# Kernel tuning notes

Measured on AMD Instinct MI355X. Metric: run time of the kernel, lower is better.

The kernel has to match this reference:

```python
import jax, jax.numpy as jnp
import numpy as np

DIM = 2048
CTX_DIM = 4096
NUM_HEADS = 16
HEAD_DIM = DIM // NUM_HEADS
EPS = 1e-6


def _rms_norm(x, weight, eps=EPS):
    # RMSNorm over last dim with learned weight (native dtype path for fp32)
    var = jnp.mean(jnp.square(x), axis=-1, keepdims=True)
    return x * jax.lax.rsqrt(var + eps) * weight


def setup_inputs() -> dict:
    key = jax.random.key(0)
    ks = jax.random.split(key, 12)
    B, L, S = 1, 8192, 512
    sd_q = 1.0 / np.sqrt(DIM)
    sd_c = 1.0 / np.sqrt(CTX_DIM)
    return {
        "x": jax.random.normal(ks[0], (B, L, DIM), dtype=jnp.float32),
        "context": jax.random.normal(ks[1], (B, S, CTX_DIM), dtype=jnp.float32),
        "Wq": jax.random.normal(ks[2], (DIM, DIM), dtype=jnp.float32) * sd_q,
        "bq": jax.random.normal(ks[3], (DIM,), dtype=jnp.float32) * 0.01,
        "Wk": jax.random.normal(ks[4], (CTX_DIM, DIM), dtype=jnp.float32) * sd_c,
        "bk": jax.random.normal(ks[5], (DIM,), dtype=jnp.float32) * 0.01,
        "Wv": jax.random.normal(ks[6], (CTX_DIM, DIM), dtype=jnp.float32) * sd_c,
        "bv": jax.random.normal(ks[7], (DIM,), dtype=jnp.float32) * 0.01,
        "Wo": jax.random.normal(ks[8], (DIM, DIM), dtype=jnp.float32) * sd_q,
        "bo": jax.random.normal(ks[9], (DIM,), dtype=jnp.float32) * 0.01,
        "g_q": jnp.ones((DIM,), dtype=jnp.float32),
        "g_k": jnp.ones((DIM,), dtype=jnp.float32),
    }


def reference(x, context, Wq, bq, Wk, bk, Wv, bv, Wo, bo, g_q, g_k):
    B, L, C = x.shape
    S = context.shape[1]
    # QKV projections + RMSNorm on Q,K (over full model dim, pre head split)
    q = _rms_norm(x @ Wq + bq, g_q)           # [B, L, C]
    k = _rms_norm(context @ Wk + bk, g_k)     # [B, S, C]
    v = context @ Wv + bv                     # [B, S, C]
    # split heads
    q = q.reshape(B, L, NUM_HEADS, HEAD_DIM)
    k = k.reshape(B, S, NUM_HEADS, HEAD_DIM)
    v = v.reshape(B, S, NUM_HEADS, HEAD_DIM)
    # non-causal SDPA
    scale = 1.0 / np.sqrt(HEAD_DIM)
    scores = jnp.einsum("blhd,bshd->bhls", q, k) * scale
    probs = jax.nn.softmax(scores, axis=-1)
    attn = jnp.einsum("bhls,bshd->blhd", probs, v).reshape(B, L, C)
    return attn @ Wo + bo
```

## Files before the change

kernel.cpp:

```cpp
#include <hip/hip_runtime.h>
#include <hip/hip_bf16.h>
#include <stdint.h>

#define L_SEQ 8192
#define S_SEQ 512
#define DIM   2048
#define CTX   4096
#define NH    16
#define HD    128

typedef __bf16 bf16_t;
typedef bf16_t bf16x8 __attribute__((ext_vector_type(8)));
typedef float  f32x4_t __attribute__((ext_vector_type(4)));
typedef float  f32x16_t __attribute__((ext_vector_type(16)));

__device__ __forceinline__ ushort f2b(float f) {
  union { float f; uint32_t u; } v; v.f = f;
  uint32_t u = v.u;
  uint32_t r = (u + 0x7fffu + ((u >> 16) & 1u)) >> 16;
  return (ushort)r;
}
__device__ __forceinline__ uint32_t pk2(float a, float b) {
  return (uint32_t)f2b(a) | ((uint32_t)f2b(b) << 16);
}
__device__ __forceinline__ float b2f(ushort u) {
  union { uint32_t u; float f; } v; v.u = ((uint32_t)u) << 16;
  return v.f;
}
__device__ __forceinline__ void gll16(const ushort* g, ushort* l) {
  __builtin_amdgcn_global_load_lds((const __attribute__((address_space(1))) void*)g,
                                   (__attribute__((address_space(3))) void*)l, 16, 0, 0);
}

__global__ __launch_bounds__(256) void k_cast(const float* __restrict__ in,
                                              ushort* __restrict__ out) {
  const size_t i = ((size_t)blockIdx.x * 256 + threadIdx.x) * 8;
  float4 a = *(const float4*)(in + i);
  float4 b = *(const float4*)(in + i + 4);
  uint4 r;
  r.x = pk2(a.x, a.y); r.y = pk2(a.z, a.w);
  r.z = pk2(b.x, b.y); r.w = pk2(b.z, b.w);
  *(uint4*)(out + i) = r;
}

__global__ __launch_bounds__(256) void k_tcast(const float* __restrict__ src,
                                               ushort* __restrict__ dst, int K, int N) {
  __shared__ float t[32][33];
  int tx = threadIdx.x, ty = threadIdx.y;
  int n0 = blockIdx.x * 32, k0 = blockIdx.y * 32;
#pragma unroll
  for (int i = 0; i < 4; i++)
    t[ty + 8 * i][tx] = src[(size_t)(k0 + ty + 8 * i) * N + n0 + tx];
  __syncthreads();
#pragma unroll
  for (int i = 0; i < 4; i++)
    dst[(size_t)(n0 + ty + 8 * i) * K + k0 + tx] = f2b(t[tx][ty + 8 * i]);
}

__global__ __launch_bounds__(256) void k_rmsnorm(const ushort* __restrict__ in,
                                                 ushort* __restrict__ out,
                                                 const float* __restrict__ g, float scale) {
  const int row = blockIdx.x, tid = threadIdx.x;
  uint4 v = *(const uint4*)(in + (size_t)row * DIM + tid * 8);
  const uint32_t* vu = (const uint32_t*)&v;
  float f[8];
#pragma unroll
  for (int i = 0; i < 4; i++) {
    f[2 * i]     = b2f((ushort)(vu[i] & 0xffffu));
    f[2 * i + 1] = b2f((ushort)(vu[i] >> 16));
  }
  float s = 0.f;
#pragma unroll
  for (int i = 0; i < 8; i++) s += f[i] * f[i];
#pragma unroll
  for (int off = 32; off; off >>= 1) s += __shfl_down(s, off);
  __shared__ float wsum[4];
  __shared__ float rtot;
  if ((tid & 63) == 0) wsum[tid >> 6] = s;
  __syncthreads();
  if (tid == 0)
    rtot = rsqrtf((wsum[0] + wsum[1] + wsum[2] + wsum[3]) * (1.0f / DIM) + 1e-6f);
  __syncthreads();
  const float rms = rtot * scale;
  const float* gp = g + tid * 8;
  float4 g0 = *(const float4*)gp, g1 = *(const float4*)(gp + 4);
  ushort r[8];
  r[0] = f2b(f[0] * rms * g0.x); r[1] = f2b(f[1] * rms * g0.y);
  r[2] = f2b(f[2] * rms * g0.z); r[3] = f2b(f[3] * rms * g0.w);
  r[4] = f2b(f[4] * rms * g1.x); r[5] = f2b(f[5] * rms * g1.y);
  r[6] = f2b(f[6] * rms * g1.z); r[7] = f2b(f[7] * rms * g1.w);
  *(uint4*)(out + (size_t)row * DIM + tid * 8) = *(uint4*)r;
}

template <int OUT_MODE>
__global__ __launch_bounds__(512, 2) void k_gemm256(const ushort* __restrict__ A,
                                                    const ushort* __restrict__ Bt,
                                                    const float* __restrict__ bias,
                                                    void* __restrict__ outp,
                                                    int M, int N, int K) {
  __shared__ __align__(16) ushort lds[65536];
  const int tid = threadIdx.x;
  const int l = tid & 63, wid = tid >> 6;
  const int wm = wid >> 2, wn = wid & 3;
  const int lr = l & 15, lq = l >> 4;

  const int nwg = gridDim.x * gridDim.y;
  const int bid = blockIdx.y * gridDim.x + blockIdx.x;
  const int swz = (bid & 7) * (nwg >> 3) + (bid >> 3);
  const int m0 = (swz / gridDim.x) * 256, n0 = (swz % gridDim.x) * 256;

  f32x4_t acc[8][4];
#pragma unroll
  for (int i = 0; i < 8; i++)
#pragma unroll
    for (int j = 0; j < 4; j++) acc[i][j] = f32x4_t{0.f, 0.f, 0.f, 0.f};

  const int srow = l >> 3;
  const int schunk = ((l & 7) ^ (srow & 7)) * 8;
  auto stage = [&](int buf, int tile, int mat, int h) {
    const ushort* gp = mat ? Bt : A;
    const int rn0 = mat ? n0 : m0;
    const size_t r0 = (size_t)(rn0 + h * 128 + wid * 8 + srow);
    const ushort* g0 = gp + r0 * K + tile * 64 + schunk;
    ushort* l0 = &lds[buf * 32768 + mat * 16384 + (h * 128 + wid * 8) * 64];
    gll16(g0, l0);
    gll16(g0 + (size_t)64 * K, l0 + 64 * 64);
  };

  auto rdA = [&](int buf, int mf, int ks) -> bf16x8 {
    const int R = wm * 128 + mf * 16 + lr;
    return *(const bf16x8*)(&lds[buf * 32768 + R * 64 + (((ks * 4 + lq) ^ (R & 7)) * 8)]);
  };
  auto rdB = [&](int buf, int nf, int ks) -> bf16x8 {
    const int R = wn * 64 + nf * 16 + lr;
    return *(const bf16x8*)(&lds[buf * 32768 + 16384 + R * 64 + (((ks * 4 + lq) ^ (R & 7)) * 8)]);
  };

  const int NT = K >> 6;
  stage(0, 0, 0, 0); stage(0, 0, 0, 1); stage(0, 0, 1, 0); stage(0, 0, 1, 1);

  bf16x8 a[4][2], a2[4][2], b[2][2], b2[2][2];
  for (int kt = 0; kt < NT; kt++) {
    const int cur = kt & 1, nxt = cur ^ 1;
    const bool pf = (kt + 1 < NT);
    if (pf) {
      stage(nxt, kt + 1, 0, 0); stage(nxt, kt + 1, 0, 1);
      stage(nxt, kt + 1, 1, 0); stage(nxt, kt + 1, 1, 1);
      asm volatile("s_waitcnt vmcnt(8)" ::: "memory");
    } else {
      asm volatile("s_waitcnt vmcnt(0)" ::: "memory");
    }
    __builtin_amdgcn_sched_barrier(0);
    __builtin_amdgcn_s_barrier();
    __builtin_amdgcn_sched_barrier(0);
#pragma unroll
    for (int mf = 0; mf < 4; mf++) { a[mf][0] = rdA(cur, mf, 0); a[mf][1] = rdA(cur, mf, 1); }
#pragma unroll
    for (int nf = 0; nf < 2; nf++) { b[nf][0] = rdB(cur, nf, 0); b[nf][1] = rdB(cur, nf, 1); }
    __builtin_amdgcn_s_setprio(1);
#pragma unroll
    for (int mf = 0; mf < 4; mf++)
#pragma unroll
      for (int nf = 0; nf < 2; nf++) {
        acc[mf][nf] = __builtin_amdgcn_mfma_f32_16x16x32_bf16(a[mf][0], b[nf][0], acc[mf][nf], 0, 0, 0);
        acc[mf][nf] = __builtin_amdgcn_mfma_f32_16x16x32_bf16(a[mf][1], b[nf][1], acc[mf][nf], 0, 0, 0);
      }
    __builtin_amdgcn_s_setprio(0);
    __builtin_amdgcn_sched_barrier(0);
    __builtin_amdgcn_s_barrier();
    __builtin_amdgcn_sched_barrier(0);
#pragma unroll
    for (int mf = 0; mf < 4; mf++) { a2[mf][0] = rdA(cur, mf + 4, 0); a2[mf][1] = rdA(cur, mf + 4, 1); }
    __builtin_amdgcn_sched_barrier(0);
    __builtin_amdgcn_s_barrier();
    __builtin_amdgcn_sched_barrier(0);
    __builtin_amdgcn_s_setprio(1);
#pragma unroll
    for (int mf = 0; mf < 4; mf++)
#pragma unroll
      for (int nf = 0; nf < 2; nf++) {
        acc[mf + 4][nf] = __builtin_amdgcn_mfma_f32_16x16x32_bf16(a2[mf][0], b[nf][0], acc[mf + 4][nf], 0, 0, 0);
        acc[mf + 4][nf] = __builtin_amdgcn_mfma_f32_16x16x32_bf16(a2[mf][1], b[nf][1], acc[mf + 4][nf], 0, 0, 0);
      }
    __builtin_amdgcn_s_setprio(0);
    __builtin_amdgcn_sched_barrier(0);
    __builtin_amdgcn_s_barrier();
    __builtin_amdgcn_sched_barrier(0);
#pragma unroll
    for (int nf = 0; nf < 2; nf++) { b2[nf][0] = rdB(cur, nf + 2, 0); b2[nf][1] = rdB(cur, nf + 2, 1); }
    __builtin_amdgcn_sched_barrier(0);
    __builtin_amdgcn_s_barrier();
    __builtin_amdgcn_sched_barrier(0);
    __builtin_amdgcn_s_setprio(1);
#pragma unroll
    for (int mf = 0; mf < 4; mf++)
#pragma unroll
      for (int nf = 0; nf < 2; nf++) {
        acc[mf + 4][nf + 2] = __builtin_amdgcn_mfma_f32_16x16x32_bf16(a2[mf][0], b2[nf][0], acc[mf + 4][nf + 2], 0, 0, 0);
        acc[mf + 4][nf + 2] = __builtin_amdgcn_mfma_f32_16x16x32_bf16(a2[mf][1], b2[nf][1], acc[mf + 4][nf + 2], 0, 0, 0);
      }
    __builtin_amdgcn_s_setprio(0);
    __builtin_amdgcn_sched_barrier(0);
    __builtin_amdgcn_s_barrier();
    __builtin_amdgcn_sched_barrier(0);
    __builtin_amdgcn_s_setprio(1);
#pragma unroll
    for (int mf = 0; mf < 4; mf++)
#pragma unroll
      for (int nf = 0; nf < 2; nf++) {
        acc[mf][nf + 2] = __builtin_amdgcn_mfma_f32_16x16x32_bf16(a[mf][0], b2[nf][0], acc[mf][nf + 2], 0, 0, 0);
        acc[mf][nf + 2] = __builtin_amdgcn_mfma_f32_16x16x32_bf16(a[mf][1], b2[nf][1], acc[mf][nf + 2], 0, 0, 0);
      }
    __builtin_amdgcn_s_setprio(0);
    __builtin_amdgcn_sched_barrier(0);
    __builtin_amdgcn_s_barrier();
    __builtin_amdgcn_sched_barrier(0);
  }

#pragma unroll
  for (int nf = 0; nf < 4; nf++) {
    const int col = n0 + wn * 64 + nf * 16 + lr;
    const float bv = bias[col];
#pragma unroll
    for (int mf = 0; mf < 8; mf++) {
#pragma unroll
      for (int r = 0; r < 4; r++) {
        const int row = m0 + wm * 128 + mf * 16 + lq * 4 + r;
        const float v = acc[mf][nf][r] + bv;
        if constexpr (OUT_MODE == 0)
          ((float*)outp)[(size_t)row * N + col] = v;
        else
          ((ushort*)outp)[(size_t)row * N + col] = f2b(v);
      }
    }
  }
}

__global__ __launch_bounds__(256) void k_gemmkv(const ushort* __restrict__ A,
                                                const ushort* __restrict__ Bt,
                                                const float* __restrict__ biasK,
                                                const float* __restrict__ biasV,
                                                ushort* __restrict__ outK,
                                                ushort* __restrict__ outVt) {
  __shared__ __align__(16) ushort As[4][128 * 32];
  __shared__ __align__(16) ushort Bs[4][64 * 32];
  const int tid = threadIdx.x;
  const int l = tid & 63, wid = tid >> 6;
  const int wr = wid >> 1, wc = wid & 1;
  const int lr = l & 15, lq = l >> 4;
  const int K = CTX, M = S_SEQ;

  const int bid = blockIdx.x;
  const int swz = (bid & 7) * 32 + (bid >> 3);
  const int n0 = (swz >> 2) * 64, m0 = (swz & 3) * 128;

  f32x4_t acc[4][2];
#pragma unroll
  for (int i = 0; i < 4; i++)
#pragma unroll
    for (int j = 0; j < 2; j++) acc[i][j] = f32x4_t{0.f, 0.f, 0.f, 0.f};

  const int srow = l >> 2;
  const int schunk = ((l & 3) ^ ((srow >> 1) & 3)) * 8;
  const ushort* gA = A  + (size_t)(m0 + srow) * K + schunk;
  const ushort* gB = Bt + (size_t)(n0 + wid * 16 + srow) * K + schunk;

  auto stage = [&](int buf, int kt) {
    const int ko = kt * 32;
    gll16(gA + (size_t)(wid * 16) * K + ko,      &As[buf][(wid * 16) * 32]);
    gll16(gA + (size_t)(64 + wid * 16) * K + ko, &As[buf][(64 + wid * 16) * 32]);
    gll16(gB + ko,                               &Bs[buf][(wid * 16) * 32]);
  };
  auto rdA = [&](int buf, int mi) -> bf16x8 {
    const int R = wr * 64 + mi * 16 + lr;
    return *(const bf16x8*)(&As[buf][R * 32 + ((lq ^ ((R >> 1) & 3)) * 8)]);
  };
  auto rdB = [&](int buf, int ni) -> bf16x8 {
    const int R = wc * 32 + ni * 16 + lr;
    return *(const bf16x8*)(&Bs[buf][R * 32 + ((lq ^ ((R >> 1) & 3)) * 8)]);
  };

  const int NT = K >> 5;
  stage(0, 0); stage(1, 1); stage(2, 2);
  for (int t = 0; t < NT; t++) {
    const int cur = t & 3;
    if (t + 3 < NT) { stage((t + 3) & 3, t + 3); asm volatile("s_waitcnt vmcnt(9)" ::: "memory"); }
    else if (t + 2 < NT) { asm volatile("s_waitcnt vmcnt(6)" ::: "memory"); }
    else if (t + 1 < NT) { asm volatile("s_waitcnt vmcnt(3)" ::: "memory"); }
    else                 { asm volatile("s_waitcnt vmcnt(0)" ::: "memory"); }
    __builtin_amdgcn_sched_barrier(0);
    __builtin_amdgcn_s_barrier();
    __builtin_amdgcn_sched_barrier(0);

    bf16x8 af[4], bfr[2];
#pragma unroll
    for (int mi = 0; mi < 4; mi++) af[mi] = rdA(cur, mi);
#pragma unroll
    for (int ni = 0; ni < 2; ni++) bfr[ni] = rdB(cur, ni);
    __builtin_amdgcn_s_setprio(1);
#pragma unroll
    for (int mi = 0; mi < 4; mi++)
#pragma unroll
      for (int ni = 0; ni < 2; ni++)
        acc[mi][ni] = __builtin_amdgcn_mfma_f32_16x16x32_bf16(af[mi], bfr[ni], acc[mi][ni], 0, 0, 0);
    __builtin_amdgcn_s_setprio(0);
    __builtin_amdgcn_sched_barrier(0);
    __builtin_amdgcn_s_barrier();
    __builtin_amdgcn_sched_barrier(0);
  }

#pragma unroll
  for (int mi = 0; mi < 4; mi++) {
#pragma unroll
    for (int ni = 0; ni < 2; ni++) {
      const int col = n0 + wc * 32 + ni * 16 + lr;
      const float bv = (col < DIM) ? biasK[col] : biasV[col - DIM];
#pragma unroll
      for (int r = 0; r < 4; r++) {
        const int row = m0 + wr * 64 + mi * 16 + lq * 4 + r;
        const float v = acc[mi][ni][r] + bv;
        if (col < DIM) outK[(size_t)row * DIM + col] = f2b(v);
        else           outVt[(size_t)(col - DIM) * M + row] = f2b(v);
      }
    }
  }
}

__global__ __launch_bounds__(256) void k_attn(const ushort* __restrict__ Qb,
                                              const ushort* __restrict__ Kb,
                                              const ushort* __restrict__ Vt,
                                              ushort* __restrict__ Ob) {
  __shared__ __align__(16) ushort smem[16384];
  ushort* Ks = smem;
  ushort* Vs = smem + 64 * 128;

  const int tid = threadIdx.x;
  const int l = tid & 63, wid = tid >> 6;
  const int lo = l & 31, hi = l >> 5;

  const int bid = blockIdx.x;
  const int swz = (bid & 7) * 128 + (bid >> 3);
  const int h = swz >> 6;
  const int q0 = (swz & 63) * 128 + wid * 32;

  bf16x8 qf[8];
  {
    const ushort* qp = Qb + (size_t)(q0 + lo) * DIM + h * HD + hi * 8;
#pragma unroll
    for (int ds = 0; ds < 8; ds++) qf[ds] = *(const bf16x8*)(qp + ds * 16);
  }

  f32x16_t o[4] = {};
  float m_run = -1e30f, l_run = 0.f;

  for (int kvb = 0; kvb < S_SEQ / 64; kvb++) {
    __syncthreads();
#pragma unroll
    for (int i = 0; i < 4; i++) {
      const int c = i * 256 + tid, row = c >> 4, cs = c & 15;
      gll16(Kb + (size_t)(kvb * 64 + row) * DIM + h * HD + ((cs ^ (row & 7)) * 8),
            Ks + c * 8);
    }
#pragma unroll
    for (int i = 0; i < 4; i++) {
      const int c = i * 256 + tid, row = c >> 3, cs = c & 7;
      gll16(Vt + (size_t)(h * HD + row) * S_SEQ + kvb * 64 + ((cs ^ (row & 7)) * 8),
            Vs + c * 8);
    }
    __syncthreads();

    f32x16_t sA = {}, sB = {};
#pragma unroll
    for (int ds = 0; ds < 8; ds++) {
      const int ch = ((hi + ds * 2) ^ (lo & 7)) * 8;
      bf16x8 kA = *(const bf16x8*)(Ks + lo * 128 + ch);
      bf16x8 kB = *(const bf16x8*)(Ks + (32 + lo) * 128 + ch);
      sA = __builtin_amdgcn_mfma_f32_32x32x16_bf16(kA, qf[ds], sA, 0, 0, 0);
      sB = __builtin_amdgcn_mfma_f32_32x32x16_bf16(kB, qf[ds], sB, 0, 0, 0);
    }

    float p[32];
#pragma unroll
    for (int i = 0; i < 16; i++) { p[i] = sA[i]; p[16 + i] = sB[i]; }
    float pm = p[0];
#pragma unroll
    for (int i = 1; i < 32; i++) pm = fmaxf(pm, p[i]);
    pm = fmaxf(pm, __shfl_xor(pm, 32));
    const float mn = fmaxf(m_run, pm);
    const float corr = __expf(m_run - mn);
    m_run = mn;
    float ps = 0.f;
#pragma unroll
    for (int i = 0; i < 32; i++) { p[i] = __expf(p[i] - mn); ps += p[i]; }
    ps += __shfl_xor(ps, 32);
    l_run = l_run * corr + ps;
#pragma unroll
    for (int nt = 0; nt < 4; nt++) o[nt] *= corr;

    uint32_t c[16];
#pragma unroll
    for (int j = 0; j < 16; j++) c[j] = pk2(p[2 * j], p[2 * j + 1]);
    bf16x8 pf[4];
#pragma unroll
    for (int s = 0; s < 4; s++) {
      const uint32_t ca = c[4 * s], cb = c[4 * s + 1], cc = c[4 * s + 2], cd = c[4 * s + 3];
      const uint32_t sa = __shfl_xor(ca, 32), sb = __shfl_xor(cb, 32);
      const uint32_t sc = __shfl_xor(cc, 32), sd = __shfl_xor(cd, 32);
      union { uint32_t u[4]; bf16x8 v; } f;
      f.u[0] = hi ? sc : ca; f.u[1] = hi ? sd : cb;
      f.u[2] = hi ? cc : sa; f.u[3] = hi ? cd : sb;
      pf[s] = f.v;
    }

#pragma unroll
    for (int nt = 0; nt < 4; nt++) {
      const int vrow = nt * 32 + lo;
#pragma unroll
      for (int s = 0; s < 4; s++) {
        bf16x8 vf = *(const bf16x8*)(Vs + vrow * 64 + (((s * 2 + hi) ^ (lo & 7)) * 8));
        o[nt] = __builtin_amdgcn_mfma_f32_32x32x16_bf16(vf, pf[s], o[nt], 0, 0, 0);
      }
    }
  }

  const float inv = 1.0f / l_run;
#pragma unroll
  for (int nt = 0; nt < 4; nt++) o[nt] *= inv;

  __syncthreads();
  float* tb = (float*)smem + wid * (32 * 33);
  const int q2 = l >> 1, dh = (l & 1) * 16;
#pragma unroll
  for (int nt = 0; nt < 4; nt++) {
#pragma unroll
    for (int r = 0; r < 16; r++)
      tb[lo * 33 + ((r & 3) + 8 * (r >> 2) + 4 * hi)] = o[nt][r];
    asm volatile("s_waitcnt lgkmcnt(0)" ::: "memory");
    __builtin_amdgcn_sched_barrier(0);
    ushort tmp[16];
#pragma unroll
    for (int j = 0; j < 16; j++) tmp[j] = f2b(tb[q2 * 33 + dh + j]);
    asm volatile("s_waitcnt lgkmcnt(0)" ::: "memory");
    __builtin_amdgcn_sched_barrier(0);
    const size_t oaddr = (size_t)(q0 + q2) * DIM + h * HD + nt * 32 + dh;
    *(uint4*)(Ob + oaddr) = *(uint4*)tmp;
    *(uint4*)(Ob + oaddr + 8) = *(uint4*)(tmp + 8);
  }
}

extern "C" void kernel_launch(void* const* d_in, const int* in_sizes, int n_in,
                              void* d_out, int out_size, void* d_ws, size_t ws_size,
                              hipStream_t stream) {
  const float* x   = (const float*)d_in[0];
  const float* ctx = (const float*)d_in[1];
  const float* Wq  = (const float*)d_in[2];
  const float* bq  = (const float*)d_in[3];
  const float* Wk  = (const float*)d_in[4];
  const float* bk  = (const float*)d_in[5];
  const float* Wv  = (const float*)d_in[6];
  const float* bv  = (const float*)d_in[7];
  const float* Wo  = (const float*)d_in[8];
  const float* bo  = (const float*)d_in[9];
  const float* gq  = (const float*)d_in[10];
  const float* gk  = (const float*)d_in[11];

  char* ws = (char*)d_ws;
  ushort* wqt   = (ushort*)(ws);
  ushort* wkt   = (ushort*)(ws + 8388608);
  ushort* wvt   = (ushort*)(ws + 25165824);
  ushort* wot   = (ushort*)(ws + 41943040);
  ushort* qb    = (ushort*)(ws + 50331648);
  ushort* kb    = (ushort*)(ws + 83886080);
  ushort* vt    = (ushort*)(ws + 85983232);
  ushort* xb    = (ushort*)(ws + 88080384);
  ushort* ctxb  = (ushort*)(ws + 88080384);
  ushort* qraw  = (ushort*)(ws + 121634816);
  ushort* kraw  = (ushort*)(ws + 121634816);
  ushort* attnb = (ushort*)(ws + 121634816);

  k_cast<<<L_SEQ * DIM / 8 / 256, 256, 0, stream>>>(x, xb);
  k_tcast<<<dim3(DIM / 32, DIM / 32), dim3(32, 8), 0, stream>>>(Wq, wqt, DIM, DIM);
  k_tcast<<<dim3(DIM / 32, CTX / 32), dim3(32, 8), 0, stream>>>(Wk, wkt, CTX, DIM);
  k_tcast<<<dim3(DIM / 32, CTX / 32), dim3(32, 8), 0, stream>>>(Wv, wvt, CTX, DIM);
  k_tcast<<<dim3(DIM / 32, DIM / 32), dim3(32, 8), 0, stream>>>(Wo, wot, DIM, DIM);

  k_gemm256<1><<<dim3(DIM / 256, L_SEQ / 256), 512, 0, stream>>>(xb, wqt, bq, qraw, L_SEQ, DIM, DIM);
  k_cast<<<S_SEQ * CTX / 8 / 256, 256, 0, stream>>>(ctx, ctxb);
  k_rmsnorm<<<L_SEQ, 256, 0, stream>>>(qraw, qb, gq, 0.08838834764831843f);
  k_gemmkv<<<256, 256, 0, stream>>>(ctxb, wkt, bk, bv, kraw, vt);
  k_rmsnorm<<<S_SEQ, 256, 0, stream>>>(kraw, kb, gk, 1.0f);
  k_attn<<<L_SEQ / 128 * NH, 256, 0, stream>>>(qb, kb, vt, attnb);
  k_gemm256<0><<<dim3(DIM / 256, L_SEQ / 256), 512, 0, stream>>>(attnb, wot, bo, d_out, L_SEQ, DIM, DIM);
}
```

Before: 338.4 us.

## Fuse fp32-to-bf16 cast of x into Q GEMM and double-buffer attention KV

The Q projection GEMM now reads fp32 x directly through registers, converts it to bf16 and writes it into LDS, so the separate cast kernel and its bf16 round trip through global memory go away. The attention kernel double-buffers its K/V tiles in LDS, prefetching the next block while the current one is computed. The price is extra register pressure and fp32 global traffic in the GEMM's A path, plus twice the LDS per attention block, which could lower occupancy.

Result: slower. 663.8 us (+96.2%).

```diff
diff --git a/kernel.cpp b/kernel.cpp
--- a/kernel.cpp
+++ b/kernel.cpp
@@ -92,7 +92,7 @@
   *(uint4*)(out + (size_t)row * DIM + tid * 8) = *(uint4*)r;
 }
 
-template <int OUT_MODE>
+template <int OUT_MODE, int AF32>
 __global__ __launch_bounds__(512, 2) void k_gemm256(const ushort* __restrict__ A,
                                                     const ushort* __restrict__ Bt,
                                                     const float* __restrict__ bias,
@@ -126,6 +126,27 @@
     gll16(g0, l0);
     gll16(g0 + (size_t)64 * K, l0 + 64 * 64);
   };
+  float4 ar[8];
+  auto loadA = [&](int tile) {
+    const float* Af = (const float*)A;
+#pragma unroll
+    for (int i = 0; i < 4; i++) {
+      const float* p = Af + (size_t)(m0 + i * 64 + wid * 8 + srow) * K + tile * 64 + schunk;
+      ar[2 * i]     = *(const float4*)p;
+      ar[2 * i + 1] = *(const float4*)(p + 4);
+    }
+  };
+  auto writeA = [&](int buf) {
+#pragma unroll
+    for (int i = 0; i < 4; i++) {
+      uint4 w;
+      w.x = pk2(ar[2 * i].x, ar[2 * i].y);
+      w.y = pk2(ar[2 * i].z, ar[2 * i].w);
+      w.z = pk2(ar[2 * i + 1].x, ar[2 * i + 1].y);
+      w.w = pk2(ar[2 * i + 1].z, ar[2 * i + 1].w);
+      *(uint4*)(&lds[buf * 32768 + (i * 64 + wid * 8 + srow) * 64 + (l & 7) * 8]) = w;
+    }
+  };
 
   auto rdA = [&](int buf, int mf, int ks) -> bf16x8 {
     const int R = wm * 128 + mf * 16 + lr;
@@ -137,18 +158,37 @@
   };
 
   const int NT = K >> 6;
-  stage(0, 0, 0, 0); stage(0, 0, 0, 1); stage(0, 0, 1, 0); stage(0, 0, 1, 1);
+  if constexpr (AF32) {
+    loadA(0);
+    stage(0, 0, 1, 0); stage(0, 0, 1, 1);
+    asm volatile("s_waitcnt vmcnt(4)" ::: "memory");
+    writeA(0);
+    asm volatile("s_waitcnt lgkmcnt(0)" ::: "memory");
+    __builtin_amdgcn_sched_barrier(0);
+  } else {
+    stage(0, 0, 0, 0); stage(0, 0, 0, 1); stage(0, 0, 1, 0); stage(0, 0, 1, 1);
+  }
 
   bf16x8 a[4][2], a2[4][2], b[2][2], b2[2][2];
   for (int kt = 0; kt < NT; kt++) {
     const int cur = kt & 1, nxt = cur ^ 1;
     const bool pf = (kt + 1 < NT);
-    if (pf) {
-      stage(nxt, kt + 1, 0, 0); stage(nxt, kt + 1, 0, 1);
-      stage(nxt, kt + 1, 1, 0); stage(nxt, kt + 1, 1, 1);
-      asm volatile("s_waitcnt vmcnt(8)" ::: "memory");
+    if constexpr (AF32) {
+      if (pf) {
+        loadA(kt + 1);
+        stage(nxt, kt + 1, 1, 0); stage(nxt, kt + 1, 1, 1);
+        asm volatile("s_waitcnt vmcnt(12)" ::: "memory");
+      } else {
+        asm volatile("s_waitcnt vmcnt(0)" ::: "memory");
+      }
     } else {
-      asm volatile("s_waitcnt vmcnt(0)" ::: "memory");
+      if (pf) {
+        stage(nxt, kt + 1, 0, 0); stage(nxt, kt + 1, 0, 1);
+        stage(nxt, kt + 1, 1, 0); stage(nxt, kt + 1, 1, 1);
+        asm volatile("s_waitcnt vmcnt(8)" ::: "memory");
+      } else {
+        asm volatile("s_waitcnt vmcnt(0)" ::: "memory");
+      }
     }
     __builtin_amdgcn_sched_barrier(0);
     __builtin_amdgcn_s_barrier();
@@ -203,6 +243,13 @@
     __builtin_amdgcn_sched_barrier(0);
     __builtin_amdgcn_s_barrier();
     __builtin_amdgcn_sched_barrier(0);
+    if constexpr (AF32) {
+      if (pf) {
+        asm volatile("s_waitcnt vmcnt(4)" ::: "memory");
+        __builtin_amdgcn_sched_barrier(0);
+        writeA(nxt);
+      }
+    }
     __builtin_amdgcn_s_setprio(1);
 #pragma unroll
     for (int mf = 0; mf < 4; mf++)
@@ -212,6 +259,9 @@
         acc[mf][nf + 2] = __builtin_amdgcn_mfma_f32_16x16x32_bf16(a[mf][1], b2[nf][1], acc[mf][nf + 2], 0, 0, 0);
       }
     __builtin_amdgcn_s_setprio(0);
+    if constexpr (AF32) {
+      asm volatile("s_waitcnt lgkmcnt(0)" ::: "memory");
+    }
     __builtin_amdgcn_sched_barrier(0);
     __builtin_amdgcn_s_barrier();
     __builtin_amdgcn_sched_barrier(0);
@@ -330,9 +380,7 @@
                                               const ushort* __restrict__ Kb,
                                               const ushort* __restrict__ Vt,
                                               ushort* __restrict__ Ob) {
-  __shared__ __align__(16) ushort smem[16384];
-  ushort* Ks = smem;
-  ushort* Vs = smem + 64 * 128;
+  __shared__ __align__(16) ushort smem[32768];
 
   const int tid = threadIdx.x;
   const int l = tid & 63, wid = tid >> 6;
@@ -353,21 +401,34 @@
   f32x16_t o[4] = {};
   float m_run = -1e30f, l_run = 0.f;
 
-  for (int kvb = 0; kvb < S_SEQ / 64; kvb++) {
-    __syncthreads();
+  auto stageKV = [&](int kvb, int buf) {
+    ushort* Ksb = smem + buf * 16384;
+    ushort* Vsb = Ksb + 8192;
 #pragma unroll
     for (int i = 0; i < 4; i++) {
       const int c = i * 256 + tid, row = c >> 4, cs = c & 15;
       gll16(Kb + (size_t)(kvb * 64 + row) * DIM + h * HD + ((cs ^ (row & 7)) * 8),
-            Ks + c * 8);
+            Ksb + c * 8);
     }
 #pragma unroll
     for (int i = 0; i < 4; i++) {
       const int c = i * 256 + tid, row = c >> 3, cs = c & 7;
       gll16(Vt + (size_t)(h * HD + row) * S_SEQ + kvb * 64 + ((cs ^ (row & 7)) * 8),
-            Vs + c * 8);
-    }
-    __syncthreads();
+            Vsb + c * 8);
+    }
+  };
+
+  stageKV(0, 0);
+  for (int kvb = 0; kvb < S_SEQ / 64; kvb++) {
+    const int cur = kvb & 1;
+    asm volatile("s_waitcnt vmcnt(0)" ::: "memory");
+    __builtin_amdgcn_sched_barrier(0);
+    __builtin_amdgcn_s_barrier();
+    __builtin_amdgcn_sched_barrier(0);
+    if (kvb + 1 < S_SEQ / 64) stageKV(kvb + 1, cur ^ 1);
+
+    const ushort* Ks = smem + cur * 16384;
+    const ushort* Vs = Ks + 8192;
 
     f32x16_t sA = {}, sB = {};
 #pragma unroll
@@ -472,23 +533,23 @@
   ushort* qb    = (ushort*)(ws + 50331648);
   ushort* kb    = (ushort*)(ws + 83886080);
   ushort* vt    = (ushort*)(ws + 85983232);
-  ushort* xb    = (ushort*)(ws + 88080384);
   ushort* ctxb  = (ushort*)(ws + 88080384);
   ushort* qraw  = (ushort*)(ws + 121634816);
   ushort* kraw  = (ushort*)(ws + 121634816);
   ushort* attnb = (ushort*)(ws + 121634816);
 
-  k_cast<<<L_SEQ * DIM / 8 / 256, 256, 0, stream>>>(x, xb);
   k_tcast<<<dim3(DIM / 32, DIM / 32), dim3(32, 8), 0, stream>>>(Wq, wqt, DIM, DIM);
   k_tcast<<<dim3(DIM / 32, CTX / 32), dim3(32, 8), 0, stream>>>(Wk, wkt, CTX, DIM);
   k_tcast<<<dim3(DIM / 32, CTX / 32), dim3(32, 8), 0, stream>>>(Wv, wvt, CTX, DIM);
   k_tcast<<<dim3(DIM / 32, DIM / 32), dim3(32, 8), 0, stream>>>(Wo, wot, DIM, DIM);
-
-  k_gemm256<1><<<dim3(DIM / 256, L_SEQ / 256), 512, 0, stream>>>(xb, wqt, bq, qraw, L_SEQ, DIM, DIM);
   k_cast<<<S_SEQ * CTX / 8 / 256, 256, 0, stream>>>(ctx, ctxb);
+
+  k_gemm256<1, 1><<<dim3(DIM / 256, L_SEQ / 256), 512, 0, stream>>>(
+      (const ushort*)x, wqt, bq, qraw, L_SEQ, DIM, DIM);
   k_rmsnorm<<<L_SEQ, 256, 0, stream>>>(qraw, qb, gq, 0.08838834764831843f);
   k_gemmkv<<<256, 256, 0, stream>>>(ctxb, wkt, bk, bv, kraw, vt);
   k_rmsnorm<<<S_SEQ, 256, 0, stream>>>(kraw, kb, gk, 1.0f);
   k_attn<<<L_SEQ / 128 * NH, 256, 0, stream>>>(qb, kb, vt, attnb);
-  k_gemm256<0><<<dim3(DIM / 256, L_SEQ / 256), 512, 0, stream>>>(attnb, wot, bo, d_out, L_SEQ, DIM, DIM);
-}
+  k_gemm256<0, 0><<<dim3(DIM / 256, L_SEQ / 256), 512, 0, stream>>>(
+      attnb, wot, bo, d_out, L_SEQ, DIM, DIM);
+}
```
